# Performance work log

Hardware: AMD Instinct MI355X
Metric: run time of the kernel (lower is better)

## Reference

```python
import jax, jax.numpy as jnp
import numpy as np

H = 2048          # hidden_size
L = 2             # num_layers
STEPS = 32        # len(action_spec)
N_ACT = 64        # uniform action_spec entry == max_actions


def setup_inputs() -> dict:
    key = jax.random.key(0)
    ks = jax.random.split(key, 8)
    s = 0.02  # small init scale to keep gates in sane range
    return {
        "start_token": jax.random.normal(ks[0], (H,), jnp.float32) * s,
        "action_emb": jax.random.normal(ks[1], (N_ACT, H), jnp.float32) * s,
        "w_ih": jax.random.normal(ks[2], (L, 4 * H, H), jnp.float32) * s,
        "w_hh": jax.random.normal(ks[3], (L, 4 * H, H), jnp.float32) * s,
        "b_ih": jax.random.normal(ks[4], (L, 4 * H), jnp.float32) * s,
        "b_hh": jax.random.normal(ks[5], (L, 4 * H), jnp.float32) * s,
        "head_w": jax.random.normal(ks[6], (STEPS, N_ACT, H), jnp.float32) * s,
        "head_b": jax.random.normal(ks[7], (STEPS, N_ACT), jnp.float32) * s,
    }


def _lstm_cell(x, h, c, w_ih_l, w_hh_l, b_ih_l, b_hh_l):
    # PyTorch LSTM gate order: i, f, g, o
    gates = w_ih_l @ x + b_ih_l + w_hh_l @ h + b_hh_l  # [4H]
    i, f, g, o = jnp.split(gates, 4)
    i = jax.nn.sigmoid(i)
    f = jax.nn.sigmoid(f)
    g = jnp.tanh(g)
    o = jax.nn.sigmoid(o)
    c_new = f * c + i * g
    h_new = o * jnp.tanh(c_new)
    return h_new, c_new


def reference(start_token, action_emb, w_ih, w_hh, b_ih, b_hh, head_w, head_b):
    n_layers = w_ih.shape[0]
    n_steps = head_w.shape[0]
    hdim = w_hh.shape[-1]
    keys = jax.random.split(jax.random.key(42), n_steps)

    h0 = jnp.zeros((n_layers, hdim), start_token.dtype)
    c0 = jnp.zeros((n_layers, hdim), start_token.dtype)

    def step(carry, xs):
        h, c, x = carry            # h, c: [L, H]; x: [H] current input token emb
        hw, hb, k = xs             # per-step head params + rng key
        hs, cs = [], []
        inp = x
        for l in range(n_layers):  # small fixed layer count
            h_l, c_l = _lstm_cell(inp, h[l], c[l], w_ih[l], w_hh[l], b_ih[l], b_hh[l])
            hs.append(h_l)
            cs.append(c_l)
            inp = h_l
        logits = hw @ inp + hb                       # [N_ACT]
        a = jax.random.categorical(k, logits)        # scalar int
        logp = jax.nn.log_softmax(logits)[a]
        nxt = action_emb[a]                          # [H]
        return (jnp.stack(hs), jnp.stack(cs), nxt), (a, logp)

    _, (actions, logps) = jax.lax.scan(step, (h0, c0, start_token), (head_w, head_b, keys))
    return actions, jnp.sum(logps)
```

## Files before the change

kernel.cpp:

```cpp
#include <hip/hip_runtime.h>

#define HDIM 2048
#define NL 2
#define NSTEPS 32
#define NACT 64
#define NBLK 256
#define TPB 512

typedef unsigned int u32;
typedef unsigned short u16;
typedef float f4 __attribute__((ext_vector_type(4)));
typedef u32 u32x4 __attribute__((ext_vector_type(4)));

__device__ __attribute__((aligned(1024))) u32 g_flags[NBLK];
__device__ __attribute__((aligned(1024))) u32 g_gen[64];

__device__ __forceinline__ void tf2x32(u32 k0, u32 k1, u32 x0, u32 x1,
                                       u32& o0, u32& o1) {
  u32 ks0 = k0, ks1 = k1, ks2 = k0 ^ k1 ^ 0x1BD11BDAu;
  x0 += ks0; x1 += ks1;
#define TF_R(r) { x0 += x1; x1 = (x1 << (r)) | (x1 >> (32 - (r))); x1 ^= x0; }
  TF_R(13) TF_R(15) TF_R(26) TF_R(6)   x0 += ks1; x1 += ks2 + 1u;
  TF_R(17) TF_R(29) TF_R(16) TF_R(24)  x0 += ks2; x1 += ks0 + 2u;
  TF_R(13) TF_R(15) TF_R(26) TF_R(6)   x0 += ks0; x1 += ks1 + 3u;
  TF_R(17) TF_R(29) TF_R(16) TF_R(24)  x0 += ks1; x1 += ks2 + 4u;
  TF_R(13) TF_R(15) TF_R(26) TF_R(6)   x0 += ks2; x1 += ks0 + 5u;
#undef TF_R
  o0 = x0; o1 = x1;
}

__device__ __forceinline__ float bflo(u32 u) { return __uint_as_float(u << 16); }
__device__ __forceinline__ float bfhi(u32 u) { return __uint_as_float(u & 0xFFFF0000u); }

__device__ __forceinline__ u16 to_bf16(float f) {
  u32 u = __float_as_uint(f);
  u += 0x7FFFu + ((u >> 16) & 1u);
  return (u16)(u >> 16);
}

struct Params {
  const float* start_token;
  const float* action_emb;
  const float* head_wT;
  const float* head_b;
  const u16*   wih;
  const u16*   whh;
  const float* bias;
  float* hbuf;
  float* part;
  float* out;
};

__device__ __forceinline__ void st_coh_f32(float* p, float v) {
  asm volatile("global_store_dword %0, %1, off sc0 sc1"
               :: "v"(p), "v"(v) : "memory");
}
__device__ __forceinline__ void st_coh_u32(u32* p, u32 v) {
  asm volatile("global_store_dword %0, %1, off sc0 sc1"
               :: "v"(p), "v"(v) : "memory");
}
__device__ __forceinline__ u32 ld_coh_u32(const u32* p) {
  u32 v;
  asm volatile("global_load_dword %0, %1, off sc0 sc1\n\ts_waitcnt vmcnt(0)"
               : "=v"(v) : "v"(p) : "memory");
  return v;
}

#define VM_DRAIN() do {                                  \
    asm volatile("s_waitcnt vmcnt(0)" ::: "memory");     \
    __builtin_amdgcn_sched_barrier(0);                   \
  } while (0)

#define BSYNC() do {                                       \
    asm volatile("s_waitcnt lgkmcnt(0)" ::: "memory");     \
    __builtin_amdgcn_s_barrier();                          \
    asm volatile("" ::: "memory");                         \
  } while (0)

__device__ __forceinline__ void load_vec(float* r, const float* __restrict__ v,
                                         int lane) {
#pragma unroll
  for (int j = 0; j < 4; ++j) {
    float4 a = *reinterpret_cast<const float4*>(v + j * 512 + lane * 8);
    float4 b = *reinterpret_cast<const float4*>(v + j * 512 + lane * 8 + 4);
    r[j * 8 + 0] = a.x; r[j * 8 + 1] = a.y; r[j * 8 + 2] = a.z; r[j * 8 + 3] = a.w;
    r[j * 8 + 4] = b.x; r[j * 8 + 5] = b.y; r[j * 8 + 6] = b.z; r[j * 8 + 7] = b.w;
  }
}

__device__ __forceinline__ void load_vec_coh(float* r, const float* v,
                                             int lane) {
  f4 t[8];
#pragma unroll
  for (int j = 0; j < 4; ++j) {
    const float* pa = v + j * 512 + lane * 8;
    const float* pb = pa + 4;
    asm volatile("global_load_dwordx4 %0, %1, off sc0 sc1"
                 : "=v"(t[2 * j + 0]) : "v"(pa) : "memory");
    asm volatile("global_load_dwordx4 %0, %1, off sc0 sc1"
                 : "=v"(t[2 * j + 1]) : "v"(pb) : "memory");
  }
  VM_DRAIN();
#pragma unroll
  for (int q = 0; q < 8; ++q) {
    r[q * 4 + 0] = t[q].x; r[q * 4 + 1] = t[q].y;
    r[q * 4 + 2] = t[q].z; r[q * 4 + 3] = t[q].w;
  }
}

__device__ __forceinline__ void issue8(const u16* const rows[8], int lane,
                                       uint4 wv[8][4]) {
#pragma unroll
  for (int r = 0; r < 8; ++r)
#pragma unroll
    for (int j = 0; j < 4; ++j)
      wv[r][j] = *reinterpret_cast<const uint4*>(rows[r] + j * 512 + lane * 8);
}

__device__ __forceinline__ float consume_row(const uint4 wvr[4],
                                             const float* xr) {
  float acc = 0.f;
#pragma unroll
  for (int j = 0; j < 4; ++j) {
    uint4 wvv = wvr[j];
    acc = fmaf(bflo(wvv.x), xr[j * 8 + 0], acc);
    acc = fmaf(bfhi(wvv.x), xr[j * 8 + 1], acc);
    acc = fmaf(bflo(wvv.y), xr[j * 8 + 2], acc);
    acc = fmaf(bfhi(wvv.y), xr[j * 8 + 3], acc);
    acc = fmaf(bflo(wvv.z), xr[j * 8 + 4], acc);
    acc = fmaf(bfhi(wvv.z), xr[j * 8 + 5], acc);
    acc = fmaf(bflo(wvv.w), xr[j * 8 + 6], acc);
    acc = fmaf(bfhi(wvv.w), xr[j * 8 + 7], acc);
  }
  return acc;
}

__device__ __forceinline__ float wave_sum(float v) {
#pragma unroll
  for (int off = 32; off > 0; off >>= 1) v += __shfl_xor(v, off);
  return v;
}

__device__ __forceinline__ void gbar(u32 target, int tid, int bid) {
  asm volatile("s_waitcnt lgkmcnt(0)" ::: "memory");
  __builtin_amdgcn_s_barrier();
  if (bid == 0) {
    if (tid < 64) {
      if (tid == 0) {
        asm volatile("s_waitcnt vmcnt(0)" ::: "memory");
        st_coh_u32(&g_flags[0], target);
      }
      const u32* fp = &g_flags[tid * 4];
      for (;;) {
        u32x4 fv;
        asm volatile(
            "global_load_dwordx4 %0, %1, off sc0 sc1\n\ts_waitcnt vmcnt(0)"
            : "=v"(fv) : "v"(fp) : "memory");
        if (__all(fv.x >= target && fv.y >= target && fv.z >= target &&
                  fv.w >= target))
          break;
        __builtin_amdgcn_s_sleep(1);
      }
      if (tid == 0) st_coh_u32(&g_gen[0], target);
    }
  } else if (tid == 0) {
    asm volatile("s_waitcnt vmcnt(0)" ::: "memory");
    st_coh_u32(&g_flags[bid], target);
    while (ld_coh_u32(&g_gen[0]) < target) __builtin_amdgcn_s_sleep(1);
  }
  __builtin_amdgcn_s_barrier();
  asm volatile("" ::: "memory");
}

__global__ void __launch_bounds__(TPB, 2) lstm_main(Params p) {
  const int tid = threadIdx.x;
  const int bid = blockIdx.x;
  const int lane = tid & 63;
  const int w = tid >> 6;
  const int m = w & 1;
  const int pairc = w >> 1;
  const int cell0 = bid * 8;

  __shared__ float part_l[8][8];
  __shared__ float gates[8][4];
  __shared__ float h1loc[8];
  __shared__ float lds_logits[NACT];

  const u16* Wl0 = (m == 0) ? p.wih : p.whh;
  const u16* Wl1 = Wl0 + (size_t)4 * HDIM * HDIM;
  const u16* rows0[8];
  const u16* rows1[8];
#pragma unroll
  for (int ci = 0; ci < 2; ++ci)
#pragma unroll
    for (int g = 0; g < 4; ++g) {
      const size_t r = (size_t)g * HDIM + cell0 + 2 * pairc + ci;
      rows0[ci * 4 + g] = Wl0 + r * HDIM;
      rows1[ci * 4 + g] = Wl1 + r * HDIM;
    }

  float b0v = 0.f, b1v = 0.f;
  if (tid < 32) {
    const int c = tid >> 2, g = tid & 3;
    b0v = p.bias[g * HDIM + cell0 + c];
    b1v = p.bias[4 * HDIM + g * HDIM + cell0 + c];
  }

  float c0 = 0.f, c1 = 0.f;
  float logp_sum = 0.f;
  int act = 0;
  u32 bt = 0;
  float vr[32];
  uint4 wv[8][4];

  issue8(rows0, lane, wv);

  for (int s = 0; s < NSTEPS; ++s) {
    const int pr = s & 1, pw = (s + 1) & 1;

    {
      if (m == 0) {
        const float* x = (s == 0) ? p.start_token
                                  : p.action_emb + (size_t)act * HDIM;
        load_vec(vr, x, lane);
      } else {
        load_vec_coh(vr, p.hbuf + (size_t)(pr * NL + 0) * HDIM, lane);
      }
      float acc[8];
#pragma unroll
      for (int r = 0; r < 8; ++r) acc[r] = consume_row(wv[r], vr);
      issue8(rows1, lane, wv);
#pragma unroll
      for (int r = 0; r < 8; ++r) {
        float v = wave_sum(acc[r]);
        if (lane == 0) part_l[w][r] = v;
      }
      BSYNC();
      if (tid < 32) {
        const int c = tid >> 2, g = tid & 3;
        const int w0 = (c >> 1) * 2, idx = (c & 1) * 4 + g;
        gates[c][g] = part_l[w0][idx] + part_l[w0 + 1][idx] + b0v;
      }
      if (tid < 8) {
        float gi = 1.f / (1.f + expf(-gates[tid][0]));
        float gf = 1.f / (1.f + expf(-gates[tid][1]));
        float gg = tanhf(gates[tid][2]);
        float go = 1.f / (1.f + expf(-gates[tid][3]));
        c0 = gf * c0 + gi * gg;
        float h = go * tanhf(c0);
        st_coh_f32(&p.hbuf[(size_t)(pw * NL + 0) * HDIM + cell0 + tid], h);
      }
      gbar(++bt, tid, bid);
    }

    {
      float hw[8];
      if (w == 0) {
        const float* hwp =
            p.head_wT + ((size_t)s * HDIM + cell0) * NACT + lane;
#pragma unroll
        for (int c = 0; c < 8; ++c) hw[c] = hwp[c * NACT];
      }
      if (m == 0)
        load_vec_coh(vr, p.hbuf + (size_t)(pw * NL + 0) * HDIM, lane);
      else
        load_vec_coh(vr, p.hbuf + (size_t)(pr * NL + 1) * HDIM, lane);
      float acc[8];
#pragma unroll
      for (int r = 0; r < 8; ++r) acc[r] = consume_row(wv[r], vr);
      if (s != NSTEPS - 1) issue8(rows0, lane, wv);
#pragma unroll
      for (int r = 0; r < 8; ++r) {
        float v = wave_sum(acc[r]);
        if (lane == 0) part_l[w][r] = v;
      }
      BSYNC();
      if (tid < 32) {
        const int c = tid >> 2, g = tid & 3;
        const int w0 = (c >> 1) * 2, idx = (c & 1) * 4 + g;
        gates[c][g] = part_l[w0][idx] + part_l[w0 + 1][idx] + b1v;
      }
      if (tid < 8) {
        float gi = 1.f / (1.f + expf(-gates[tid][0]));
        float gf = 1.f / (1.f + expf(-gates[tid][1]));
        float gg = tanhf(gates[tid][2]);
        float go = 1.f / (1.f + expf(-gates[tid][3]));
        c1 = gf * c1 + gi * gg;
        float h = go * tanhf(c1);
        st_coh_f32(&p.hbuf[(size_t)(pw * NL + 1) * HDIM + cell0 + tid], h);
        h1loc[tid] = h;
      }
      if (w == 0) {
        float a2 = 0.f;
#pragma unroll
        for (int c = 0; c < 8; ++c) a2 = fmaf(hw[c], h1loc[c], a2);
        st_coh_f32(&p.part[(size_t)lane * NBLK + bid], a2);
      }
      gbar(++bt, tid, bid);
    }

    {
      const int a = tid >> 3, j = tid & 7;
      const float* pb = p.part + (size_t)a * NBLK + j * 32;
      f4 t[8];
#pragma unroll
      for (int q = 0; q < 8; ++q) {
        const float* pq = pb + q * 4;
        asm volatile("global_load_dwordx4 %0, %1, off sc0 sc1"
                     : "=v"(t[q]) : "v"(pq) : "memory");
      }
      VM_DRAIN();
      float sum = 0.f;
#pragma unroll
      for (int q = 0; q < 8; ++q) sum += t[q].x + t[q].y + t[q].z + t[q].w;
      sum += __shfl_xor(sum, 1);
      sum += __shfl_xor(sum, 2);
      sum += __shfl_xor(sum, 4);
      if (j == 0) lds_logits[a] = sum;
    }
    BSYNC();

    {
      float logit = lds_logits[lane] + p.head_b[s * NACT + lane];

      u32 kA, kB;
      tf2x32(0u, 42u, 0u, (u32)s, kA, kB);
      u32 y0, y1;
      tf2x32(kA, kB, 0u, (u32)lane, y0, y1);
      u32 bits = y0 ^ y1;

      float uf = __uint_as_float(0x3f800000u | (bits >> 9)) - 1.0f;
      const float tiny = 1.17549435e-38f;
      float u = fmaxf(tiny, uf + tiny);
      float gum = -logf(-logf(u));

      float score = logit + gum;
      int bi = lane;
      float bs = score;
#pragma unroll
      for (int off = 32; off > 0; off >>= 1) {
        float os = __shfl_xor(bs, off);
        int oi = __shfl_xor(bi, off);
        if (os > bs || (os == bs && oi < bi)) { bs = os; bi = oi; }
      }
      float mx = logit;
#pragma unroll
      for (int off = 32; off > 0; off >>= 1) mx = fmaxf(mx, __shfl_xor(mx, off));
      float se = wave_sum(expf(logit - mx));
      float la = __shfl(logit, bi);
      logp_sum += la - mx - logf(se);
      act = bi;
      if (bid == 0 && tid == 0) p.out[s] = (float)bi;
    }
  }
  if (bid == 0 && tid == 0) p.out[NSTEPS] = logp_sum;
}

__global__ void init_kernel(const float* __restrict__ wih,
                            const float* __restrict__ whh,
                            const float* __restrict__ bih,
                            const float* __restrict__ bhh,
                            const float* __restrict__ head_w,
                            u16* __restrict__ wih_bf, u16* __restrict__ whh_bf,
                            float* __restrict__ head_wT,
                            float* __restrict__ bias, float* __restrict__ hbuf) {
  const size_t idx = (size_t)blockIdx.x * blockDim.x + threadIdx.x;
  const size_t stride = (size_t)gridDim.x * blockDim.x;
  const size_t n4 = (size_t)NL * 4 * HDIM * HDIM / 4;
  for (size_t k = idx; k < n4; k += stride) {
    float4 a = reinterpret_cast<const float4*>(wih)[k];
    float4 b = reinterpret_cast<const float4*>(whh)[k];
    ushort4 ua, ub;
    ua.x = to_bf16(a.x); ua.y = to_bf16(a.y);
    ua.z = to_bf16(a.z); ua.w = to_bf16(a.w);
    ub.x = to_bf16(b.x); ub.y = to_bf16(b.y);
    ub.z = to_bf16(b.z); ub.w = to_bf16(b.w);
    reinterpret_cast<ushort4*>(wih_bf)[k] = ua;
    reinterpret_cast<ushort4*>(whh_bf)[k] = ub;
  }
  for (size_t k = idx; k < (size_t)NSTEPS * HDIM * NACT; k += stride) {
    const int a = (int)(k & (NACT - 1));
    const int h = (int)((k >> 6) & (HDIM - 1));
    const int s = (int)(k >> 17);
    head_wT[k] = head_w[((size_t)s * NACT + a) * HDIM + h];
  }
  for (size_t k = idx; k < (size_t)NL * 4 * HDIM; k += stride)
    bias[k] = bih[k] + bhh[k];
  for (size_t k = idx; k < (size_t)2 * NL * HDIM; k += stride) hbuf[k] = 0.f;
  for (size_t k = idx; k < NBLK; k += stride) g_flags[k] = 0u;
  for (size_t k = idx; k < 64; k += stride) g_gen[k] = 0u;
}

extern "C" void kernel_launch(void* const* d_in, const int* in_sizes, int n_in,
                              void* d_out, int out_size, void* d_ws,
                              size_t ws_size, hipStream_t stream) {
  (void)in_sizes; (void)n_in; (void)out_size; (void)ws_size;
  const float* start_token = (const float*)d_in[0];
  const float* action_emb  = (const float*)d_in[1];
  const float* w_ih        = (const float*)d_in[2];
  const float* w_hh        = (const float*)d_in[3];
  const float* b_ih        = (const float*)d_in[4];
  const float* b_hh        = (const float*)d_in[5];
  const float* head_w      = (const float*)d_in[6];
  const float* head_b      = (const float*)d_in[7];

  char* ws = (char*)d_ws;
  const size_t WN = (size_t)NL * 4 * HDIM * HDIM;
  u16* wih_bf    = (u16*)ws;
  u16* whh_bf    = (u16*)(ws + WN * 2);
  size_t off     = WN * 4;
  float* head_wT = (float*)(ws + off); off += (size_t)NSTEPS * HDIM * NACT * 4;
  float* bias    = (float*)(ws + off); off += (size_t)NL * 4 * HDIM * 4;
  float* hbuf    = (float*)(ws + off); off += (size_t)2 * NL * HDIM * 4;
  float* partb   = (float*)(ws + off); off += (size_t)NACT * NBLK * 4;

  init_kernel<<<dim3(2048), dim3(256), 0, stream>>>(
      w_ih, w_hh, b_ih, b_hh, head_w, wih_bf, whh_bf, head_wT, bias, hbuf);

  Params p;
  p.start_token = start_token;
  p.action_emb = action_emb;
  p.head_wT = head_wT;
  p.head_b = head_b;
  p.wih = wih_bf;
  p.whh = whh_bf;
  p.bias = bias;
  p.hbuf = hbuf;
  p.part = partb;
  p.out = (float*)d_out;

  lstm_main<<<dim3(NBLK), dim3(TPB), 0, stream>>>(p);
}
```

Measured before the change: 2.332 ms.

## Stream weight rows in quarter chunks instead of prefetching full layer

Replaces the full 32-register-vector weight prefetch per layer with a rolling one-quarter buffer. Each quarter is consumed and the next one issued, so only the first quarter of the next layer is prefetched across the grid barrier. This cuts VGPR pressure, but most weight loads now sit on the critical path after the barrier instead of overlapping with it. It also adds spin iteration caps to the grid barrier and makes the wave index uniform through readfirstlane.

```diff
diff --git a/kernel.cpp b/kernel.cpp
--- a/kernel.cpp
+++ b/kernel.cpp
@@ -6,6 +6,7 @@
 #define NACT 64
 #define NBLK 256
 #define TPB 512
+#define SPIN_MAX (1 << 20)
 
 typedef unsigned int u32;
 typedef unsigned short u16;
@@ -108,31 +109,30 @@
   }
 }
 
-__device__ __forceinline__ void issue8(const u16* const rows[8], int lane,
-                                       uint4 wv[8][4]) {
-#pragma unroll
-  for (int r = 0; r < 8; ++r)
-#pragma unroll
-    for (int j = 0; j < 4; ++j)
-      wv[r][j] = *reinterpret_cast<const uint4*>(rows[r] + j * 512 + lane * 8);
-}
-
-__device__ __forceinline__ float consume_row(const uint4 wvr[4],
-                                             const float* xr) {
-  float acc = 0.f;
-#pragma unroll
-  for (int j = 0; j < 4; ++j) {
-    uint4 wvv = wvr[j];
-    acc = fmaf(bflo(wvv.x), xr[j * 8 + 0], acc);
-    acc = fmaf(bfhi(wvv.x), xr[j * 8 + 1], acc);
-    acc = fmaf(bflo(wvv.y), xr[j * 8 + 2], acc);
-    acc = fmaf(bfhi(wvv.y), xr[j * 8 + 3], acc);
-    acc = fmaf(bflo(wvv.z), xr[j * 8 + 4], acc);
-    acc = fmaf(bfhi(wvv.z), xr[j * 8 + 5], acc);
-    acc = fmaf(bflo(wvv.w), xr[j * 8 + 6], acc);
-    acc = fmaf(bfhi(wvv.w), xr[j * 8 + 7], acc);
-  }
-  return acc;
+__device__ __forceinline__ void issue_q(const u16* const rows[8], int j,
+                                        int lane, u32x4 q[8]) {
+#pragma unroll
+  for (int r = 0; r < 8; ++r) {
+    const u16* ptr = rows[r] + j * 512 + lane * 8;
+    asm volatile("global_load_dwordx4 %0, %1, off"
+                 : "=v"(q[r]) : "v"(ptr));
+  }
+}
+
+__device__ __forceinline__ void consume_q(const u32x4 q[8], const float* xr,
+                                          int j, float acc[8]) {
+#pragma unroll
+  for (int r = 0; r < 8; ++r) {
+    u32x4 wvv = q[r];
+    acc[r] = fmaf(bflo(wvv.x), xr[j * 8 + 0], acc[r]);
+    acc[r] = fmaf(bfhi(wvv.x), xr[j * 8 + 1], acc[r]);
+    acc[r] = fmaf(bflo(wvv.y), xr[j * 8 + 2], acc[r]);
+    acc[r] = fmaf(bfhi(wvv.y), xr[j * 8 + 3], acc[r]);
+    acc[r] = fmaf(bflo(wvv.z), xr[j * 8 + 4], acc[r]);
+    acc[r] = fmaf(bfhi(wvv.z), xr[j * 8 + 5], acc[r]);
+    acc[r] = fmaf(bflo(wvv.w), xr[j * 8 + 6], acc[r]);
+    acc[r] = fmaf(bfhi(wvv.w), xr[j * 8 + 7], acc[r]);
+  }
 }
 
 __device__ __forceinline__ float wave_sum(float v) {
@@ -151,6 +151,7 @@
         st_coh_u32(&g_flags[0], target);
       }
       const u32* fp = &g_flags[tid * 4];
+      int it = 0;
       for (;;) {
         u32x4 fv;
         asm volatile(
@@ -159,6 +160,7 @@
         if (__all(fv.x >= target && fv.y >= target && fv.z >= target &&
                   fv.w >= target))
           break;
+        if (++it > SPIN_MAX) break;
         __builtin_amdgcn_s_sleep(1);
       }
       if (tid == 0) st_coh_u32(&g_gen[0], target);
@@ -166,7 +168,11 @@
   } else if (tid == 0) {
     asm volatile("s_waitcnt vmcnt(0)" ::: "memory");
     st_coh_u32(&g_flags[bid], target);
-    while (ld_coh_u32(&g_gen[0]) < target) __builtin_amdgcn_s_sleep(1);
+    int it = 0;
+    while (ld_coh_u32(&g_gen[0]) < target) {
+      if (++it > SPIN_MAX) break;
+      __builtin_amdgcn_s_sleep(1);
+    }
   }
   __builtin_amdgcn_s_barrier();
   asm volatile("" ::: "memory");
@@ -176,9 +182,10 @@
   const int tid = threadIdx.x;
   const int bid = blockIdx.x;
   const int lane = tid & 63;
-  const int w = tid >> 6;
-  const int m = w & 1;
-  const int pairc = w >> 1;
+  const int wu = __builtin_amdgcn_readfirstlane(tid >> 6);
+  const int w = wu;
+  const int m = wu & 1;
+  const int pairc = wu >> 1;
   const int cell0 = bid * 8;
 
   __shared__ float part_l[8][8];
@@ -211,9 +218,9 @@
   int act = 0;
   u32 bt = 0;
   float vr[32];
-  uint4 wv[8][4];
-
-  issue8(rows0, lane, wv);
+  u32x4 qA[8];
+
+  issue_q(rows0, 0, lane, qA);
 
   for (int s = 0; s < NSTEPS; ++s) {
     const int pr = s & 1, pw = (s + 1) & 1;
@@ -228,8 +235,14 @@
       }
       float acc[8];
 #pragma unroll
-      for (int r = 0; r < 8; ++r) acc[r] = consume_row(wv[r], vr);
-      issue8(rows1, lane, wv);
+      for (int r = 0; r < 8; ++r) acc[r] = 0.f;
+#pragma unroll
+      for (int j = 0; j < 4; ++j) {
+        VM_DRAIN();
+        consume_q(qA, vr, j, acc);
+        if (j < 3) issue_q(rows0, j + 1, lane, qA);
+      }
+      issue_q(rows1, 0, lane, qA);
 #pragma unroll
       for (int r = 0; r < 8; ++r) {
         float v = wave_sum(acc[r]);
@@ -267,8 +280,15 @@
         load_vec_coh(vr, p.hbuf + (size_t)(pr * NL + 1) * HDIM, lane);
       float acc[8];
 #pragma unroll
-      for (int r = 0; r < 8; ++r) acc[r] = consume_row(wv[r], vr);
-      if (s != NSTEPS - 1) issue8(rows0, lane, wv);
+      for (int r = 0; r < 8; ++r) acc[r] = 0.f;
+#pragma unroll
+      for (int j = 0; j < 4; ++j) {
+        VM_DRAIN();
+        consume_q(qA, vr, j, acc);
+        if (j < 3) issue_q(rows1, j + 1, lane, qA);
+      }
+      if (s != NSTEPS - 1)
+        issue_q(rows0, 0, lane, qA);
 #pragma unroll
       for (int r = 0; r < 8; ++r) {
         float v = wave_sum(acc[r]);
```

After: 2.004 ms. 1.16x faster.
